# Kernel optimization log

Hardware: AMD Instinct MI355X
Metric: run time of the kernel (lower is better)

The kernel has to match this reference:

```python
import jax, jax.numpy as jnp
import numpy as np

TD = 256  # text_dim


def conv1x1(x, w, b):
    # 1x1 conv == per-pixel matmul over channels; w: [out,in], x: [B,C,H,W]
    return jnp.einsum('oc,bchw->bohw', w, x) + b[None, :, None, None]


def setup_inputs() -> dict:
    key = jax.random.key(0)
    ks = iter(jax.random.split(key, 48))
    B = 4
    cin = [64, 128, 256, 512]
    vshapes = [(B, 64, 64, 64), (B, 128, 32, 32), (B, 256, 16, 16), (B, 512, 8, 8)]
    tshapes = [(B, TD, 64, 64), (B, TD, 32, 32), (B, TD, 16, 16), (B, TD, 8, 8)]
    d = {}
    for i, s in enumerate(vshapes):
        d[f'v{i}'] = jax.random.normal(next(ks), s, jnp.float32)
    for i, s in enumerate(tshapes):
        d[f't{i}'] = jax.random.normal(next(ks), s, jnp.float32)
    for i in range(4):
        d[f'vp_w{i}'] = jax.random.normal(next(ks), (TD, cin[i]), jnp.float32) / np.float32(np.sqrt(cin[i]))
        d[f'vp_b{i}'] = jnp.zeros((TD,), jnp.float32)
        d[f'op_w{i}'] = jax.random.normal(next(ks), (cin[i], TD), jnp.float32) / np.float32(np.sqrt(TD))
        d[f'op_b{i}'] = jnp.zeros((cin[i],), jnp.float32)
    for nm in ['q', 'k', 'v']:
        d[f'{nm}_w'] = jax.random.normal(next(ks), (TD, TD), jnp.float32) / np.float32(np.sqrt(TD))
        d[f'{nm}_b'] = jnp.zeros((TD,), jnp.float32)
    d['sg_w'] = jax.random.normal(next(ks), (TD, 4 * TD), jnp.float32) / np.float32(np.sqrt(4 * TD))
    d['sg_b'] = jnp.zeros((TD,), jnp.float32)
    d['bn_g'] = jnp.ones((TD,), jnp.float32)
    d['bn_b'] = jnp.zeros((TD,), jnp.float32)
    d['fc1_w'] = jax.random.normal(next(ks), (1024, TD), jnp.float32) / np.float32(np.sqrt(TD))
    d['fc1_b'] = jnp.zeros((1024,), jnp.float32)
    d['fc2_w'] = jax.random.normal(next(ks), (2048, 1024), jnp.float32) / np.float32(np.sqrt(1024))
    d['fc2_b'] = jnp.zeros((2048,), jnp.float32)
    return d


def reference(v0, v1, v2, v3, t0, t1, t2, t3,
              vp_w0, vp_b0, op_w0, op_b0,
              vp_w1, vp_b1, op_w1, op_b1,
              vp_w2, vp_b2, op_w2, op_b2,
              vp_w3, vp_b3, op_w3, op_b3,
              q_w, q_b, k_w, k_b, v_w, v_b,
              sg_w, sg_b, bn_g, bn_b, fc1_w, fc1_b, fc2_w, fc2_b):
    vs = [v0, v1, v2, v3]
    ts = [t0, t1, t2, t3]
    vpw = [vp_w0, vp_w1, vp_w2, vp_w3]
    vpb = [vp_b0, vp_b1, vp_b2, vp_b3]
    opw = [op_w0, op_w1, op_w2, op_w3]
    opb = [op_b0, op_b1, op_b2, op_b3]
    scale = np.float32(1.0 / np.sqrt(TD))

    enhanced = []
    for i in range(4):
        vp = conv1x1(vs[i], vpw[i], vpb[i])          # [B,TD,H,W]
        q = conv1x1(vp, q_w, q_b)
        k = conv1x1(ts[i], k_w, k_b)
        v = conv1x1(ts[i], v_w, v_b)
        B, C, H, W = vp.shape
        qf = q.reshape(B, C, H * W)                  # [B,C,Nq]
        kf = k.reshape(B, C, -1)                     # [B,C,Nk]
        vf = v.reshape(B, C, -1)                     # [B,C,Nk]
        attn = jax.nn.softmax(jnp.einsum('bcn,bcm->bnm', qf, kf) * scale, axis=-1)  # [B,Nq,Nk]
        av = jnp.einsum('bcm,bnm->bcn', vf, attn).reshape(B, C, H, W)
        enhanced.append(conv1x1(av, opw[i], opb[i]) + vs[i])

    # align text maps to smallest spatial size (divisible -> block average pool)
    s = ts[3].shape[2]
    pooled = [t.reshape(t.shape[0], t.shape[1], s, t.shape[2] // s, s, t.shape[3] // s).mean(axis=(3, 5))
              for t in ts]
    cat = jnp.concatenate(pooled, axis=1)            # [B,4*TD,s,s]
    x = conv1x1(cat, sg_w, sg_b)                     # [B,TD,s,s]
    # BatchNorm2d, training mode (batch statistics, biased variance)
    mu = x.mean(axis=(0, 2, 3), keepdims=True)
    var = x.var(axis=(0, 2, 3), keepdims=True)
    x = (x - mu) * jax.lax.rsqrt(var + 1e-5) * bn_g[None, :, None, None] + bn_b[None, :, None, None]
    x = jax.nn.relu(x).mean(axis=(2, 3))             # global avg pool -> [B,TD]
    x = jax.nn.relu(x @ fc1_w.T + fc1_b)
    x = x @ fc2_w.T + fc2_b                          # [B,2048]
    semantic = x.reshape(-1, 2, 1024)
    return (semantic, enhanced[0], enhanced[1], enhanced[2], enhanced[3])
```

## Files before the change

### kernel.cpp

```cpp
#include <hip/hip_runtime.h>

typedef __bf16 bf16_t;
typedef bf16_t bf16x8 __attribute__((ext_vector_type(8)));
typedef float f32x4 __attribute__((ext_vector_type(4)));
typedef unsigned short u16;
typedef unsigned long long u64;

__device__ __forceinline__ u16 f2bf(float f) {
  union { float f; unsigned u; } v; v.f = f;
  unsigned r = v.u + 0x7FFFu + ((v.u >> 16) & 1u);
  return (u16)(r >> 16);
}
__device__ __forceinline__ bf16x8 ld8(const u16* p) {
  return *reinterpret_cast<const bf16x8*>(p);
}
__device__ __forceinline__ void gload_lds16(const void* g, void* l) {
  __builtin_amdgcn_global_load_lds(
      (const __attribute__((address_space(1))) void*)g,
      (__attribute__((address_space(3))) void*)l, 16, 0, 0);
}

struct Ptrs4 { const float* p[4]; };

struct CvtJob { const float* s; u16* d; int n; };
struct CvtJobs { CvtJob j[8]; };

__global__ __launch_bounds__(256) void cvt_multi(CvtJobs jobs) {
  CvtJob J = jobs.j[blockIdx.y];
  for (int i = blockIdx.x * 256 + threadIdx.x; i < J.n; i += gridDim.x * 256)
    J.d[i] = f2bf(J.s[i]);
}

struct TJob { const float* s; u16* d; int C, N, nbx, nbz, off; };
struct TJobs { TJob j[12]; };

__global__ __launch_bounds__(256) void transpose_batch(TJobs J, int nj) {
  int bid = blockIdx.x, ji = 0;
#pragma unroll
  for (int k = 1; k < 12; ++k)
    if (k < nj && bid >= J.j[k].off) ji = k;
  TJob job = J.j[ji];
  int local = bid - job.off;
  int z = local % job.nbz;
  int l2 = local / job.nbz;
  int bx = l2 % job.nbx, by = l2 / job.nbx;
  __shared__ float t[32][33];
  int tx = threadIdx.x & 31, ty = threadIdx.x >> 5;
  int n0 = bx * 32, c0 = by * 32;
  long zi = (long)z * job.C * job.N, zo = (long)z * job.N * job.C;
#pragma unroll
  for (int i = 0; i < 4; ++i)
    t[ty + 8 * i][tx] = job.s[zi + (long)(c0 + ty + 8 * i) * job.N + n0 + tx];
  __syncthreads();
#pragma unroll
  for (int i = 0; i < 4; ++i)
    job.d[zo + (long)(n0 + ty + 8 * i) * job.C + c0 + tx] = f2bf(t[tx][ty + 8 * i]);
}

struct GJob {
  const u16 *A, *X;
  const float *bias, *bias2;
  void *o1, *o2;
  const float* res;
  int M, N, K, nbx, nbz, off, mode;
};
struct GJobs { GJob j[8]; };

__global__ __launch_bounds__(256) void gemm_batch(GJobs J, int nj) {
  int bid = blockIdx.x, ji = 0;
#pragma unroll
  for (int k = 1; k < 8; ++k)
    if (k < nj && bid >= J.j[k].off) ji = k;
  GJob job = J.j[ji];
  int local = bid - job.off;
  const int z = local % job.nbz;
  int l2 = local / job.nbz;
  const int n0 = (l2 % job.nbx) * 64, m0 = (l2 / job.nbx) * 64;
  const int M = job.M, N = job.N, K = job.K;
  const u16* __restrict__ A = job.A;
  const u16* __restrict__ X = job.X;

  __shared__ __attribute__((aligned(16))) u16 As[64][40];
  __shared__ __attribute__((aligned(16))) u16 Bs[64][40];
  const int tid = threadIdx.x;
  const long Xz = (long)z * N * K;
  const int arow = tid >> 2, acol = (tid & 3) * 8;
  const int w = tid >> 6, lane = tid & 63, g = lane >> 4, ln = lane & 15;
  const int wm = (w >> 1) * 32, wn = (w & 1) * 32;
  f32x4 zero = {0.f, 0.f, 0.f, 0.f};
  f32x4 acc[2][2];
#pragma unroll
  for (int i = 0; i < 2; ++i)
#pragma unroll
    for (int j = 0; j < 2; ++j) acc[i][j] = zero;

  for (int k0 = 0; k0 < K; k0 += 32) {
    int4 av = *reinterpret_cast<const int4*>(A + (long)(m0 + arow) * K + k0 + acol);
    int4 bv = *reinterpret_cast<const int4*>(X + Xz + (long)(n0 + arow) * K + k0 + acol);
    __syncthreads();
    *reinterpret_cast<int4*>(&As[arow][acol]) = av;
    *reinterpret_cast<int4*>(&Bs[arow][acol]) = bv;
    __syncthreads();
    bf16x8 a0 = ld8(&As[wm + ln][g * 8]);
    bf16x8 a1 = ld8(&As[wm + 16 + ln][g * 8]);
    bf16x8 b0 = ld8(&Bs[wn + ln][g * 8]);
    bf16x8 b1 = ld8(&Bs[wn + 16 + ln][g * 8]);
    acc[0][0] = __builtin_amdgcn_mfma_f32_16x16x32_bf16(a0, b0, acc[0][0], 0, 0, 0);
    acc[0][1] = __builtin_amdgcn_mfma_f32_16x16x32_bf16(a0, b1, acc[0][1], 0, 0, 0);
    acc[1][0] = __builtin_amdgcn_mfma_f32_16x16x32_bf16(a1, b0, acc[1][0], 0, 0, 0);
    acc[1][1] = __builtin_amdgcn_mfma_f32_16x16x32_bf16(a1, b1, acc[1][1], 0, 0, 0);
  }

#pragma unroll
  for (int i = 0; i < 2; ++i) {
#pragma unroll
    for (int j = 0; j < 2; ++j) {
      int mr0 = m0 + wm + 16 * i + g * 4;
      int nc = n0 + wn + 16 * j + ln;
      if (job.mode == 0) {
        u64 pk = 0;
#pragma unroll
        for (int r = 0; r < 4; ++r) {
          float val = acc[i][j][r] + (job.bias ? job.bias[mr0 + r] : 0.f);
          pk |= (u64)f2bf(val) << (16 * r);
        }
        *reinterpret_cast<u64*>((u16*)job.o1 + ((long)z * N + nc) * M + mr0) = pk;
      } else if (job.mode == 1) {
#pragma unroll
        for (int r = 0; r < 4; ++r) {
          float val = acc[i][j][r] + (job.bias ? job.bias[mr0 + r] : 0.f);
          ((u16*)job.o1)[((long)z * M + mr0 + r) * N + nc] = f2bf(val);
        }
      } else if (job.mode == 2) {
#pragma unroll
        for (int r = 0; r < 4; ++r) {
          long idx = ((long)z * M + mr0 + r) * N + nc;
          float val = acc[i][j][r] + job.bias[mr0 + r];
          if (job.res) val += job.res[idx];
          ((float*)job.o1)[idx] = val;
        }
      } else {
        long tbase = (long)z * N * 256 + (long)(nc >> 5) * 8192;
        if (mr0 < 256) {
          u64 pk = 0;
#pragma unroll
          for (int r = 0; r < 4; ++r)
            pk |= (u64)f2bf(acc[i][j][r] + job.bias[mr0 + r]) << (16 * r);
          int byteoff = ((nc & 31) * 512 + mr0 * 2) ^ ((nc & 7) << 4);
          *reinterpret_cast<u64*>((char*)job.o1 + tbase * 2 + byteoff) = pk;
        } else {
          int d0 = mr0 - 256;
#pragma unroll
          for (int r = 0; r < 4; ++r) {
            int d = d0 + r;
            int byteoff = (d * 64 + (nc & 31) * 2) ^ ((d & 7) << 4);
            *reinterpret_cast<u16*>((char*)job.o2 + tbase * 2 + byteoff) =
                f2bf(acc[i][j][r] + job.bias2[d]);
          }
        }
      }
    }
  }
}

struct AJob { const u16 *Q, *K, *V; u16* O; int N, off; };
struct AJobs { AJob j[4]; };

__global__ __launch_bounds__(128, 2) void attn_batch(AJobs J, int nj) {
  __shared__ __attribute__((aligned(16))) char stKV[2][2][16384];
  __shared__ __attribute__((aligned(16))) u16 Ps[2][32][40];
  int bid = blockIdx.x, ji = 0;
#pragma unroll
  for (int k = 1; k < 4; ++k)
    if (k < nj && bid >= J.j[k].off) ji = k;
  AJob job = J.j[ji];
  int local = bid - job.off;
  const int N = job.N;
  const int nbx = N >> 6;
  int z, bx;
  if (nbx >= 2) {
    z = (local & 7) >> 1;
    bx = ((local >> 3) << 1) | (local & 1);
  } else {
    z = local & 3;
    bx = 0;
  }
  const int tid = threadIdx.x;
  const int w = tid >> 6, lane = tid & 63;
  const int g = lane >> 4, ln = lane & 15;
  const float scale = 0.0625f;
  const int nt = N >> 5;
  const long tb = (long)z * nt;
  const int qbase = bx * 64 + w * 32;

  bf16x8 qf[2][8];
#pragma unroll
  for (int qh = 0; qh < 2; ++qh) {
    const u16* qp = job.Q + ((long)z * N + qbase + qh * 16 + ln) * 256 + g * 8;
#pragma unroll
    for (int cc = 0; cc < 8; ++cc) qf[qh][cc] = ld8(qp + cc * 32);
  }
  f32x4 zero = {0.f, 0.f, 0.f, 0.f};
  f32x4 oacc[16][2];
#pragma unroll
  for (int ct = 0; ct < 16; ++ct) {
    oacc[ct][0] = zero;
    oacc[ct][1] = zero;
  }
  float mrow[2] = {-1e30f, -1e30f}, lrow[2] = {0.f, 0.f};

  const char* gsrc = (const char*)(w ? job.V : job.K);
  auto stage_tile = [&](int buf, int t) {
    const char* gp = gsrc + (tb + t) * 16384 + lane * 16;
    char* lp = &stKV[buf][w][0];
#pragma unroll
    for (int q = 0; q < 16; ++q) gload_lds16(gp + q * 1024, lp + q * 1024);
  };

  stage_tile(0, 0);
  asm volatile("s_waitcnt vmcnt(0)" ::: "memory");
  __syncthreads();

  const int swz = (ln & 7) << 4;
  for (int t = 0; t < nt; ++t) {
    const int buf = t & 1;
    if (t + 1 < nt) stage_tile(buf ^ 1, t + 1);
    const char* Kb = &stKV[buf][0][0];
    const char* Vb = &stKV[buf][1][0];

    f32x4 s[2][2];
    s[0][0] = zero; s[0][1] = zero; s[1][0] = zero; s[1][1] = zero;
#pragma unroll
    for (int cc = 0; cc < 8; ++cc) {
      bf16x8 k0 = *reinterpret_cast<const bf16x8*>(Kb + ((ln * 512 + cc * 64 + g * 16) ^ swz));
      bf16x8 k1 = *reinterpret_cast<const bf16x8*>(Kb + (((16 + ln) * 512 + cc * 64 + g * 16) ^ swz));
      s[0][0] = __builtin_amdgcn_mfma_f32_16x16x32_bf16(k0, qf[0][cc], s[0][0], 0, 0, 0);
      s[0][1] = __builtin_amdgcn_mfma_f32_16x16x32_bf16(k0, qf[1][cc], s[0][1], 0, 0, 0);
      s[1][0] = __builtin_amdgcn_mfma_f32_16x16x32_bf16(k1, qf[0][cc], s[1][0], 0, 0, 0);
      s[1][1] = __builtin_amdgcn_mfma_f32_16x16x32_bf16(k1, qf[1][cc], s[1][1], 0, 0, 0);
    }
#pragma unroll
    for (int qh = 0; qh < 2; ++qh) {
      float x[8];
#pragma unroll
      for (int r = 0; r < 4; ++r) { x[r] = s[0][qh][r] * scale; x[4 + r] = s[1][qh][r] * scale; }
      float lm = fmaxf(fmaxf(fmaxf(x[0], x[1]), fmaxf(x[2], x[3])),
                       fmaxf(fmaxf(x[4], x[5]), fmaxf(x[6], x[7])));
      lm = fmaxf(lm, __shfl_xor(lm, 16));
      lm = fmaxf(lm, __shfl_xor(lm, 32));
      if (!__all(lm - mrow[qh] <= 8.0f)) {
        float nm = fmaxf(mrow[qh], lm);
        float fac = __expf(mrow[qh] - nm);
        mrow[qh] = nm;
        lrow[qh] *= fac;
#pragma unroll
        for (int ct = 0; ct < 16; ++ct)
#pragma unroll
          for (int r = 0; r < 4; ++r) oacc[ct][qh][r] *= fac;
      }
      float ps = 0.f;
#pragma unroll
      for (int j2 = 0; j2 < 8; ++j2) { x[j2] = __expf(x[j2] - mrow[qh]); ps += x[j2]; }
      ps += __shfl_xor(ps, 16);
      ps += __shfl_xor(ps, 32);
      lrow[qh] += ps;
      u64 plo = (u64)f2bf(x[0]) | ((u64)f2bf(x[1]) << 16) |
                ((u64)f2bf(x[2]) << 32) | ((u64)f2bf(x[3]) << 48);
      u64 phi = (u64)f2bf(x[4]) | ((u64)f2bf(x[5]) << 16) |
                ((u64)f2bf(x[6]) << 32) | ((u64)f2bf(x[7]) << 48);
      *reinterpret_cast<u64*>(&Ps[w][qh * 16 + ln][g * 4]) = plo;
      *reinterpret_cast<u64*>(&Ps[w][qh * 16 + ln][16 + g * 4]) = phi;
    }
    asm volatile("s_waitcnt lgkmcnt(0)" ::: "memory");
    bf16x8 pa0 = ld8(&Ps[w][ln][g * 8]);
    bf16x8 pa1 = ld8(&Ps[w][16 + ln][g * 8]);
#pragma unroll
    for (int ct = 0; ct < 16; ++ct) {
      bf16x8 vv = *reinterpret_cast<const bf16x8*>(
          Vb + (((ct * 16 + ln) * 64 + g * 16) ^ swz));
      oacc[ct][0] = __builtin_amdgcn_mfma_f32_16x16x32_bf16(vv, pa0, oacc[ct][0], 0, 0, 0);
      oacc[ct][1] = __builtin_amdgcn_mfma_f32_16x16x32_bf16(vv, pa1, oacc[ct][1], 0, 0, 0);
    }
    asm volatile("s_waitcnt vmcnt(0)" ::: "memory");
    __syncthreads();
  }

#pragma unroll
  for (int qh = 0; qh < 2; ++qh) {
    const float rl = 1.f / lrow[qh];
    u16* Oz = job.O + ((long)z * N + qbase + qh * 16 + ln) * 256;
#pragma unroll
    for (int ct = 0; ct < 16; ++ct) {
      u64 pk = 0;
#pragma unroll
      for (int r = 0; r < 4; ++r) pk |= (u64)f2bf(oacc[ct][qh][r] * rl) << (16 * r);
      *reinterpret_cast<u64*>(Oz + ct * 16 + g * 4) = pk;
    }
  }
}

__global__ __launch_bounds__(256) void qeb_k(const float* __restrict__ qw,
                                             const float* __restrict__ qb, Ptrs4 vpb,
                                             float* __restrict__ qeb) {
  int o = threadIdx.x;
  int lvl = blockIdx.x;
  const float* vb = vpb.p[lvl];
  float acc = qb[o];
  for (int k = 0; k < 256; ++k) acc += qw[o * 256 + k] * vb[k];
  qeb[lvl * 256 + o] = acc;
}

__global__ __launch_bounds__(256) void pool_k(Ptrs4 ts, u16* __restrict__ poolT) {
  int gt = blockIdx.x * 256 + threadIdx.x;
  int ch = gt & 1023;
  int pix = (gt >> 10) & 63;
  int b = gt >> 16;
  int level = ch >> 8, c = ch & 255;
  int H = 64 >> level;
  int f = H >> 3;
  int py = pix >> 3, px = pix & 7;
  const float* src = ts.p[level] + (((long)b * 256 + c) * H + py * f) * H + px * f;
  float s = 0.f;
  for (int dy = 0; dy < f; ++dy)
    for (int dx = 0; dx < f; ++dx) s += src[dy * H + dx];
  poolT[gt] = f2bf(s / (float)(f * f));
}

__global__ __launch_bounds__(64) void bn_k(const float* __restrict__ x,
                                           const float* __restrict__ gw,
                                           const float* __restrict__ gb,
                                           float* __restrict__ xp) {
  int ch = blockIdx.x, t = threadIdx.x;
  float v[4], s = 0.f, sq = 0.f;
#pragma unroll
  for (int b = 0; b < 4; ++b) {
    v[b] = x[((long)b * 256 + ch) * 64 + t];
    s += v[b];
    sq += v[b] * v[b];
  }
#pragma unroll
  for (int off = 32; off; off >>= 1) {
    s += __shfl_xor(s, off);
    sq += __shfl_xor(sq, off);
  }
  float mu = s * (1.f / 256.f);
  float var = sq * (1.f / 256.f) - mu * mu;
  float rstd = rsqrtf(var + 1e-5f);
  float G = gw[ch], Bb = gb[ch];
#pragma unroll
  for (int b = 0; b < 4; ++b) {
    float y = fmaxf((v[b] - mu) * rstd * G + Bb, 0.f);
#pragma unroll
    for (int off = 32; off; off >>= 1) y += __shfl_xor(y, off);
    if (t == 0) xp[b * 256 + ch] = y * (1.f / 64.f);
  }
}

__global__ __launch_bounds__(256) void fc1_k(const float* __restrict__ xp,
                                             const float* __restrict__ w,
                                             const float* __restrict__ bias,
                                             float* __restrict__ o1) {
  int gt = blockIdx.x * 256 + threadIdx.x;
  int b = gt >> 10, j = gt & 1023;
  float acc = bias[j];
  const float* wr = w + (long)j * 256;
  const float* xr = xp + b * 256;
  for (int k = 0; k < 256; ++k) acc += xr[k] * wr[k];
  o1[gt] = fmaxf(acc, 0.f);
}

__global__ __launch_bounds__(256) void fc2_k(const float* __restrict__ o1,
                                             const float* __restrict__ w,
                                             const float* __restrict__ bias,
                                             float* __restrict__ out) {
  int gt = blockIdx.x * 256 + threadIdx.x;
  int b = gt >> 11, o = gt & 2047;
  float acc = bias[o];
  const float* wr = w + (long)o * 1024;
  const float* xr = o1 + b * 1024;
  for (int k = 0; k < 1024; ++k) acc += xr[k] * wr[k];
  out[gt] = acc;
}

extern "C" void kernel_launch(void* const* d_in, const int* in_sizes, int n_in,
                              void* d_out, int out_size, void* d_ws, size_t ws_size,
                              hipStream_t stream) {
  (void)in_sizes; (void)n_in; (void)out_size; (void)ws_size;
  const float *v_in[4], *t_in[4], *vp_w[4], *vp_b[4], *op_w[4], *op_b[4];
  for (int i = 0; i < 4; ++i) {
    v_in[i] = (const float*)d_in[i];
    t_in[i] = (const float*)d_in[4 + i];
    vp_w[i] = (const float*)d_in[8 + 4 * i];
    vp_b[i] = (const float*)d_in[9 + 4 * i];
    op_w[i] = (const float*)d_in[10 + 4 * i];
    op_b[i] = (const float*)d_in[11 + 4 * i];
  }
  const float* q_w = (const float*)d_in[24];
  const float* q_b = (const float*)d_in[25];
  const float* k_w = (const float*)d_in[26];
  const float* k_b = (const float*)d_in[27];
  const float* v_w = (const float*)d_in[28];
  const float* v_b = (const float*)d_in[29];
  const float* sg_w = (const float*)d_in[30];
  const float* sg_b = (const float*)d_in[31];
  const float* bn_g = (const float*)d_in[32];
  const float* bn_b = (const float*)d_in[33];
  const float* fc1_w = (const float*)d_in[34];
  const float* fc1_b = (const float*)d_in[35];
  const float* fc2_w = (const float*)d_in[36];
  const float* fc2_b = (const float*)d_in[37];
  float* out = (float*)d_out;

  const int cin[4] = {64, 128, 256, 512};
  const int NN[4] = {4096, 1024, 256, 64};
  const long NOFF[4] = {0, 4194304, 5242880, 5505024};
  const long VOFF[4] = {0, 1048576, 1572864, 1835008};

  char* ws = (char*)d_ws;
  size_t off = 0;
  auto alloc = [&](size_t bytes) {
    void* p = ws + off;
    off += (bytes + 255) & ~(size_t)255;
    return p;
  };
  u16* w_q = (u16*)alloc(65536 * 2);
  u16* w_kv = (u16*)alloc(131072 * 2);
  u16* w_op[4];
  for (int i = 0; i < 4; ++i) w_op[i] = (u16*)alloc((size_t)cin[i] * 256 * 2);
  u16* w_sg = (u16*)alloc(262144 * 2);
  u16* vpwT[4];
  for (int i = 0; i < 4; ++i) vpwT[i] = (u16*)alloc((size_t)cin[i] * 256 * 2);
  u16* qe[4];
  for (int i = 0; i < 4; ++i) qe[i] = (u16*)alloc((size_t)256 * cin[i] * 2);
  float* qeb = (float*)alloc(1024 * 4);
  u16* vT = (u16*)alloc((size_t)1966080 * 2);
  u16* tT = (u16*)alloc((size_t)5570560 * 2);
  u16* QT = (u16*)alloc((size_t)5570560 * 2);
  u16* Kt = (u16*)alloc((size_t)5570560 * 2);
  u16* Vt = (u16*)alloc((size_t)5570560 * 2);
  u16* Ob = (u16*)alloc((size_t)5570560 * 2);
  u16* poolT = (u16*)alloc((size_t)262144 * 2);
  float* xbuf = (float*)alloc((size_t)65536 * 4);
  float* xp = (float*)alloc(1024 * 4);
  float* fc1o = (float*)alloc(4096 * 4);

  CvtJobs jobs;
  jobs.j[0] = {q_w, w_q, 65536};
  jobs.j[1] = {k_w, w_kv, 65536};
  jobs.j[2] = {v_w, w_kv + 65536, 65536};
  jobs.j[3] = {op_w[0], w_op[0], cin[0] * 256};
  jobs.j[4] = {op_w[1], w_op[1], cin[1] * 256};
  jobs.j[5] = {op_w[2], w_op[2], cin[2] * 256};
  jobs.j[6] = {op_w[3], w_op[3], cin[3] * 256};
  jobs.j[7] = {sg_w, w_sg, 262144};
  cvt_multi<<<dim3(32, 8), 256, 0, stream>>>(jobs);

  {
    TJobs T;
    int boff = 0, nj = 0;
    for (int i = 0; i < 4; ++i) {
      int nbx = cin[i] / 32;
      T.j[nj] = {vp_w[i], vpwT[i], 256, cin[i], nbx, 1, boff};
      boff += nbx * 8;
      ++nj;
    }
    for (int i = 0; i < 4; ++i) {
      int nbx = NN[i] / 32, nby = cin[i] / 32;
      T.j[nj] = {v_in[i], vT + VOFF[i], cin[i], NN[i], nbx, 4, boff};
      boff += nbx * nby * 4;
      ++nj;
    }
    for (int i = 0; i < 4; ++i) {
      int nbx = NN[i] / 32;
      T.j[nj] = {t_in[i], tT + NOFF[i], 256, NN[i], nbx, 4, boff};
      boff += nbx * 8 * 4;
      ++nj;
    }
    transpose_batch<<<boff, 256, 0, stream>>>(T, nj);
  }

  {
    GJobs G;
    int boff = 0;
    for (int i = 0; i < 4; ++i) {
      int nbx = cin[i] / 64;
      G.j[i] = {w_q, vpwT[i], nullptr, nullptr, qe[i], nullptr, nullptr,
                256, cin[i], 256, nbx, 1, boff, 1};
      boff += nbx * 4;
    }
    gemm_batch<<<boff, 256, 0, stream>>>(G, 4);
  }
  Ptrs4 vpbp;
  for (int i = 0; i < 4; ++i) vpbp.p[i] = vp_b[i];
  qeb_k<<<4, 256, 0, stream>>>(q_w, q_b, vpbp, qeb);

  {
    GJobs G;
    int boff = 0, nj = 0;
    for (int i = 0; i < 4; ++i) {
      int nbx = NN[i] / 64;
      G.j[nj] = {qe[i], vT + VOFF[i], qeb + 256 * i, nullptr, QT + NOFF[i], nullptr,
                 nullptr, 256, NN[i], cin[i], nbx, 4, boff, 0};
      boff += nbx * 4 * 4;
      ++nj;
    }
    for (int i = 0; i < 4; ++i) {
      int nbx = NN[i] / 64;
      G.j[nj] = {w_kv, tT + NOFF[i], k_b, v_b, Kt + NOFF[i], Vt + NOFF[i], nullptr,
                 512, NN[i], 256, nbx, 4, boff, 3};
      boff += nbx * 8 * 4;
      ++nj;
    }
    gemm_batch<<<boff, 256, 0, stream>>>(G, 8);
  }

  {
    AJobs A;
    int boff = 0;
    for (int i = 0; i < 4; ++i) {
      A.j[i] = {QT + NOFF[i], Kt + NOFF[i], Vt + NOFF[i], Ob + NOFF[i], NN[i], boff};
      boff += (NN[i] / 64) * 4;
    }
    attn_batch<<<boff, 128, 0, stream>>>(A, 4);
  }

  Ptrs4 tp;
  for (int i = 0; i < 4; ++i) tp.p[i] = t_in[i];
  pool_k<<<1024, 256, 0, stream>>>(tp, poolT);

  const long enh_off[4] = {8192, 8192 + 1048576, 8192 + 1048576 + 524288,
                           8192 + 1048576 + 524288 + 262144};
  {
    GJobs G;
    int boff = 0;
    for (int i = 0; i < 4; ++i) {
      int nbx = NN[i] / 64, nby = cin[i] / 64;
      G.j[i] = {w_op[i], Ob + NOFF[i], op_b[i], nullptr, out + enh_off[i], nullptr,
                v_in[i], cin[i], NN[i], 256, nbx, 4, boff, 2};
      boff += nbx * nby * 4;
    }
    G.j[4] = {w_sg, poolT, sg_b, nullptr, xbuf, nullptr, nullptr,
              256, 64, 1024, 1, 4, boff, 2};
    boff += 1 * 4 * 4;
    gemm_batch<<<boff, 256, 0, stream>>>(G, 5);
  }

  bn_k<<<256, 64, 0, stream>>>(xbuf, bn_g, bn_b, xp);
  fc1_k<<<16, 256, 0, stream>>>(xp, fc1_w, fc1_b, fc1o);
  fc2_k<<<32, 256, 0, stream>>>(fc1o, fc2_w, fc2_b, out);
}
```

Measured before the change: 468.1 us.

## Split attention KV range into two segments with a merge kernel

Attention is restructured as a split-K flash attention. Each query tile is processed by two blocks covering halves of the key/value sequence, and each writes unnormalized partial outputs plus row max and sum. A separate merge kernel then combines the two partials. Blocks grow to four waves that cooperatively stage the K/V tiles, the pipelining uses a partial vmcnt wait with raw barriers, and setprio is added around the MFMA sections. The aim is more parallelism for the long-sequence level and better load overlap, at the cost of an extra kernel launch, extra partial-output traffic, and reuse of the tT buffer as scratch.

```diff
diff --git a/kernel.cpp b/kernel.cpp
--- a/kernel.cpp
+++ b/kernel.cpp
@@ -163,58 +163,56 @@
   }
 }
 
-struct AJob { const u16 *Q, *K, *V; u16* O; int N, off; };
+struct AJob { const u16 *Q, *K, *V; long noff; int N, off; };
 struct AJobs { AJob j[4]; };
 
-__global__ __launch_bounds__(128, 2) void attn_batch(AJobs J, int nj) {
+template <int NQH>
+__global__ __launch_bounds__(256, 1) void attn_part(
+    AJobs J, int nj, u16* __restrict__ OP0, u16* __restrict__ OP1,
+    float* __restrict__ ML0, float* __restrict__ ML1) {
   __shared__ __attribute__((aligned(16))) char stKV[2][2][16384];
-  __shared__ __attribute__((aligned(16))) u16 Ps[2][32][40];
+  __shared__ __attribute__((aligned(16))) u16 Ps[4][32][40];
   int bid = blockIdx.x, ji = 0;
 #pragma unroll
   for (int k = 1; k < 4; ++k)
     if (k < nj && bid >= J.j[k].off) ji = k;
   AJob job = J.j[ji];
   int local = bid - job.off;
+  const int z = local & 3;
+  const int r2 = local >> 2;
+  const int kseg = r2 & 1, qt = r2 >> 1;
   const int N = job.N;
-  const int nbx = N >> 6;
-  int z, bx;
-  if (nbx >= 2) {
-    z = (local & 7) >> 1;
-    bx = ((local >> 3) << 1) | (local & 1);
-  } else {
-    z = local & 3;
-    bx = 0;
-  }
   const int tid = threadIdx.x;
   const int w = tid >> 6, lane = tid & 63;
   const int g = lane >> 4, ln = lane & 15;
   const float scale = 0.0625f;
-  const int nt = N >> 5;
-  const long tb = (long)z * nt;
-  const int qbase = bx * 64 + w * 32;
-
-  bf16x8 qf[2][8];
-#pragma unroll
-  for (int qh = 0; qh < 2; ++qh) {
+  const int nt = N >> 6;
+  const int qbase = qt * (NQH * 64) + w * (NQH * 16);
+
+  bf16x8 qf[NQH][8];
+#pragma unroll
+  for (int qh = 0; qh < NQH; ++qh) {
     const u16* qp = job.Q + ((long)z * N + qbase + qh * 16 + ln) * 256 + g * 8;
 #pragma unroll
     for (int cc = 0; cc < 8; ++cc) qf[qh][cc] = ld8(qp + cc * 32);
   }
   f32x4 zero = {0.f, 0.f, 0.f, 0.f};
-  f32x4 oacc[16][2];
-#pragma unroll
-  for (int ct = 0; ct < 16; ++ct) {
-    oacc[ct][0] = zero;
-    oacc[ct][1] = zero;
-  }
-  float mrow[2] = {-1e30f, -1e30f}, lrow[2] = {0.f, 0.f};
-
-  const char* gsrc = (const char*)(w ? job.V : job.K);
+  f32x4 oacc[16][NQH];
+#pragma unroll
+  for (int ct = 0; ct < 16; ++ct)
+#pragma unroll
+    for (int qh = 0; qh < NQH; ++qh) oacc[ct][qh] = zero;
+  float mrow[NQH], lrow[NQH];
+#pragma unroll
+  for (int qh = 0; qh < NQH; ++qh) { mrow[qh] = -1e30f; lrow[qh] = 0.f; }
+
+  const long kvbyte = ((long)z * (N >> 5) + (long)kseg * nt) * 16384;
+  const char* gsrc = ((w < 2) ? (const char*)job.K : (const char*)job.V) + kvbyte;
   auto stage_tile = [&](int buf, int t) {
-    const char* gp = gsrc + (tb + t) * 16384 + lane * 16;
-    char* lp = &stKV[buf][w][0];
-#pragma unroll
-    for (int q = 0; q < 16; ++q) gload_lds16(gp + q * 1024, lp + q * 1024);
+    const char* gp = gsrc + (long)t * 16384 + (w & 1) * 8192 + lane * 16;
+    char* lp = &stKV[buf][w >> 1][(w & 1) * 8192];
+#pragma unroll
+    for (int q = 0; q < 8; ++q) gload_lds16(gp + q * 1024, lp + q * 1024);
   };
 
   stage_tile(0, 0);
@@ -224,23 +222,36 @@
   const int swz = (ln & 7) << 4;
   for (int t = 0; t < nt; ++t) {
     const int buf = t & 1;
-    if (t + 1 < nt) stage_tile(buf ^ 1, t + 1);
+    if (t + 1 < nt) {
+      stage_tile(buf ^ 1, t + 1);
+      asm volatile("s_waitcnt vmcnt(8)" ::: "memory");
+    } else {
+      asm volatile("s_waitcnt vmcnt(0)" ::: "memory");
+    }
+    __builtin_amdgcn_sched_barrier(0);
+    __builtin_amdgcn_s_barrier();
     const char* Kb = &stKV[buf][0][0];
     const char* Vb = &stKV[buf][1][0];
 
-    f32x4 s[2][2];
-    s[0][0] = zero; s[0][1] = zero; s[1][0] = zero; s[1][1] = zero;
+    f32x4 s[2][NQH];
+#pragma unroll
+    for (int kh = 0; kh < 2; ++kh)
+#pragma unroll
+      for (int qh = 0; qh < NQH; ++qh) s[kh][qh] = zero;
+    __builtin_amdgcn_s_setprio(1);
 #pragma unroll
     for (int cc = 0; cc < 8; ++cc) {
       bf16x8 k0 = *reinterpret_cast<const bf16x8*>(Kb + ((ln * 512 + cc * 64 + g * 16) ^ swz));
       bf16x8 k1 = *reinterpret_cast<const bf16x8*>(Kb + (((16 + ln) * 512 + cc * 64 + g * 16) ^ swz));
-      s[0][0] = __builtin_amdgcn_mfma_f32_16x16x32_bf16(k0, qf[0][cc], s[0][0], 0, 0, 0);
-      s[0][1] = __builtin_amdgcn_mfma_f32_16x16x32_bf16(k0, qf[1][cc], s[0][1], 0, 0, 0);
-      s[1][0] = __builtin_amdgcn_mfma_f32_16x16x32_bf16(k1, qf[0][cc], s[1][0], 0, 0, 0);
-      s[1][1] = __builtin_amdgcn_mfma_f32_16x16x32_bf16(k1, qf[1][cc], s[1][1], 0, 0, 0);
-    }
-#pragma unroll
-    for (int qh = 0; qh < 2; ++qh) {
+#pragma unroll
+      for (int qh = 0; qh < NQH; ++qh) {
+        s[0][qh] = __builtin_amdgcn_mfma_f32_16x16x32_bf16(k0, qf[qh][cc], s[0][qh], 0, 0, 0);
+        s[1][qh] = __builtin_amdgcn_mfma_f32_16x16x32_bf16(k1, qf[qh][cc], s[1][qh], 0, 0, 0);
+      }
+    }
+    __builtin_amdgcn_s_setprio(0);
+#pragma unroll
+    for (int qh = 0; qh < NQH; ++qh) {
       float x[8];
 #pragma unroll
       for (int r = 0; r < 4; ++r) { x[r] = s[0][qh][r] * scale; x[4 + r] = s[1][qh][r] * scale; }
@@ -272,31 +283,71 @@
       *reinterpret_cast<u64*>(&Ps[w][qh * 16 + ln][16 + g * 4]) = phi;
     }
     asm volatile("s_waitcnt lgkmcnt(0)" ::: "memory");
-    bf16x8 pa0 = ld8(&Ps[w][ln][g * 8]);
-    bf16x8 pa1 = ld8(&Ps[w][16 + ln][g * 8]);
+    bf16x8 pa[NQH];
+#pragma unroll
+    for (int qh = 0; qh < NQH; ++qh) pa[qh] = ld8(&Ps[w][qh * 16 + ln][g * 8]);
+    __builtin_amdgcn_s_setprio(1);
 #pragma unroll
     for (int ct = 0; ct < 16; ++ct) {
       bf16x8 vv = *reinterpret_cast<const bf16x8*>(
           Vb + (((ct * 16 + ln) * 64 + g * 16) ^ swz));
-      oacc[ct][0] = __builtin_amdgcn_mfma_f32_16x16x32_bf16(vv, pa0, oacc[ct][0], 0, 0, 0);
-      oacc[ct][1] = __builtin_amdgcn_mfma_f32_16x16x32_bf16(vv, pa1, oacc[ct][1], 0, 0, 0);
-    }
-    asm volatile("s_waitcnt vmcnt(0)" ::: "memory");
-    __syncthreads();
-  }
-
-#pragma unroll
-  for (int qh = 0; qh < 2; ++qh) {
-    const float rl = 1.f / lrow[qh];
-    u16* Oz = job.O + ((long)z * N + qbase + qh * 16 + ln) * 256;
+#pragma unroll
+      for (int qh = 0; qh < NQH; ++qh)
+        oacc[ct][qh] = __builtin_amdgcn_mfma_f32_16x16x32_bf16(vv, pa[qh], oacc[ct][qh], 0, 0, 0);
+    }
+    __builtin_amdgcn_s_setprio(0);
+    __builtin_amdgcn_sched_barrier(0);
+    __builtin_amdgcn_s_barrier();
+  }
+
+  u16* OP = kseg ? OP1 : OP0;
+  float* ML = kseg ? ML1 : ML0;
+#pragma unroll
+  for (int qh = 0; qh < NQH; ++qh) {
+    const long qrow = (long)z * N + qbase + qh * 16 + ln;
+    u16* Oz = OP + job.noff + qrow * 256;
 #pragma unroll
     for (int ct = 0; ct < 16; ++ct) {
       u64 pk = 0;
 #pragma unroll
-      for (int r = 0; r < 4; ++r) pk |= (u64)f2bf(oacc[ct][qh][r] * rl) << (16 * r);
+      for (int r = 0; r < 4; ++r) pk |= (u64)f2bf(oacc[ct][qh][r]) << (16 * r);
       *reinterpret_cast<u64*>(Oz + ct * 16 + g * 4) = pk;
     }
-  }
+    if (g == 0) {
+      long mlrow = (job.noff >> 8) + qrow;
+      ML[mlrow * 2] = mrow[qh];
+      ML[mlrow * 2 + 1] = lrow[qh];
+    }
+  }
+}
+
+__global__ __launch_bounds__(256) void merge_k(
+    const u16* __restrict__ OP0, const u16* __restrict__ OP1,
+    const float* __restrict__ ML0, const float* __restrict__ ML1,
+    u16* __restrict__ Ob) {
+  const int tid = threadIdx.x;
+  const long row = (long)blockIdx.x * 8 + (tid >> 5);
+  const int c = (tid & 31) * 8;
+  float ma = ML0[row * 2], la = ML0[row * 2 + 1];
+  float mb = ML1[row * 2], lb = ML1[row * 2 + 1];
+  float M = fmaxf(ma, mb);
+  float wa = __expf(ma - M), wb = __expf(mb - M);
+  float rl = 1.f / (wa * la + wb * lb);
+  bf16x8 A = ld8(OP0 + row * 256 + c);
+  bf16x8 B = ld8(OP1 + row * 256 + c);
+  u64 pk0 = 0, pk1 = 0;
+#pragma unroll
+  for (int j = 0; j < 4; ++j) {
+    float v = (wa * (float)A[j] + wb * (float)B[j]) * rl;
+    pk0 |= (u64)f2bf(v) << (16 * j);
+  }
+#pragma unroll
+  for (int j = 0; j < 4; ++j) {
+    float v = (wa * (float)A[4 + j] + wb * (float)B[4 + j]) * rl;
+    pk1 |= (u64)f2bf(v) << (16 * j);
+  }
+  *reinterpret_cast<u64*>(Ob + row * 256 + c) = pk0;
+  *reinterpret_cast<u64*>(Ob + row * 256 + c + 4) = pk1;
 }
 
 __global__ __launch_bounds__(256) void qeb_k(const float* __restrict__ qw,
@@ -415,6 +466,7 @@
   const int NN[4] = {4096, 1024, 256, 64};
   const long NOFF[4] = {0, 4194304, 5242880, 5505024};
   const long VOFF[4] = {0, 1048576, 1572864, 1835008};
+  const long TOTROWS = 21760;
 
   char* ws = (char*)d_ws;
   size_t off = 0;
@@ -439,10 +491,14 @@
   u16* Kt = (u16*)alloc((size_t)5570560 * 2);
   u16* Vt = (u16*)alloc((size_t)5570560 * 2);
   u16* Ob = (u16*)alloc((size_t)5570560 * 2);
+  u16* OP1 = (u16*)alloc((size_t)5570560 * 2);
+  float* ML0 = (float*)alloc((size_t)TOTROWS * 2 * 4);
+  float* ML1 = (float*)alloc((size_t)TOTROWS * 2 * 4);
   u16* poolT = (u16*)alloc((size_t)262144 * 2);
   float* xbuf = (float*)alloc((size_t)65536 * 4);
   float* xp = (float*)alloc(1024 * 4);
   float* fc1o = (float*)alloc(4096 * 4);
+  u16* OP0 = tT;
 
   CvtJobs jobs;
   jobs.j[0] = {q_w, w_q, 65536};
@@ -517,11 +573,15 @@
   {
     AJobs A;
     int boff = 0;
-    for (int i = 0; i < 4; ++i) {
-      A.j[i] = {QT + NOFF[i], Kt + NOFF[i], Vt + NOFF[i], Ob + NOFF[i], NN[i], boff};
-      boff += (NN[i] / 64) * 4;
-    }
-    attn_batch<<<boff, 128, 0, stream>>>(A, 4);
+    for (int i = 0; i < 3; ++i) {
+      A.j[i] = {QT + NOFF[i], Kt + NOFF[i], Vt + NOFF[i], NOFF[i], NN[i], boff};
+      boff += (NN[i] / 128) * 8;
+    }
+    attn_part<2><<<boff, 256, 0, stream>>>(A, 3, OP0, OP1, ML0, ML1);
+    AJobs B;
+    B.j[0] = {QT + NOFF[3], Kt + NOFF[3], Vt + NOFF[3], NOFF[3], 64, 0};
+    attn_part<1><<<8, 256, 0, stream>>>(B, 1, OP0, OP1, ML0, ML1);
+    merge_k<<<TOTROWS / 8, 256, 0, stream>>>(OP0, OP1, ML0, ML1, Ob);
   }
 
   Ptrs4 tp;
```

After: 396.9 us. 1.18x faster.
